# Performance work log

Measured on AMD Instinct MI355X. Metric: run time of the kernel, lower is better.

Reference implementation:

```python
import math
import jax, jax.numpy as jnp
import numpy as np

CAPACITY_FACTOR = 1.0
MIN_CAPACITY = 4


def setup_inputs() -> dict:
    key = jax.random.key(0)
    k1, k2 = jax.random.split(key)
    x = jax.random.normal(k1, (8192, 1024), dtype=jnp.float32)
    wg = jax.random.normal(k2, (1024, 64), dtype=jnp.float32) * 0.02
    return {"x": x, "wg": wg}


def reference(x, wg):
    # Gate projection: [S, D] @ [D, E] -> [S, E]
    logits = x @ wg
    S, E = logits.shape
    # _capacity: ceil(S / E * capacity_factor * 2) for top-2, floored at min_capacity (static)
    capacity = max(math.ceil((S / E) * (CAPACITY_FACTOR * 2.0)), MIN_CAPACITY)

    gates = jax.nn.softmax(logits, axis=-1)           # [S, E]
    org_gates = gates

    # top-1 expert
    indices1_s = jnp.argmax(gates, axis=1)
    mask1 = jax.nn.one_hot(indices1_s, E, dtype=jnp.int32)
    # top-2 expert (deterministic: no gumbel sampling)
    logits_except1 = jnp.where(mask1.astype(bool), -jnp.inf, logits)
    indices2_s = jnp.argmax(logits_except1, axis=1)
    mask2 = jax.nn.one_hot(indices2_s, E, dtype=jnp.int32)

    # per-expert running positions
    locations1 = jnp.cumsum(mask1, axis=0) - 1        # [S, E]
    locations2 = jnp.cumsum(mask2, axis=0) - 1 + jnp.sum(mask1, axis=0, keepdims=True)

    # load-balancing aux loss
    me = jnp.mean(gates, axis=0)
    ce = jnp.mean(mask1.astype(gates.dtype), axis=0)
    l_aux = jnp.sum(me * ce) * E * E

    exp_counts = jnp.sum(mask1 + mask2, axis=0)

    # drop tokens over capacity
    mask1 = mask1 * (locations1 < capacity).astype(jnp.int32)
    mask2 = mask2 * (locations2 < capacity).astype(jnp.int32)

    locations1_s = jnp.sum(locations1 * mask1, axis=1)  # [S]
    locations2_s = jnp.sum(locations2 * mask2, axis=1)

    mask1_f = mask1.astype(gates.dtype)
    mask2_f = mask2.astype(gates.dtype)
    gates1_s = jnp.sum(gates * mask1_f, axis=1)
    gates2_s = jnp.sum(gates * mask2_f, axis=1)
    denom_s = jnp.clip(gates1_s + gates2_s, jnp.finfo(gates.dtype).eps)
    gates1_s = gates1_s / denom_s
    gates2_s = gates2_s / denom_s

    gates1 = gates1_s[:, None] * mask1_f              # [S, E]
    gates2 = gates2_s[:, None] * mask2_f

    locations1_sc = jax.nn.one_hot(locations1_s, capacity, dtype=gates.dtype)  # [S, C]
    locations2_sc = jax.nn.one_hot(locations2_s, capacity, dtype=gates.dtype)

    combine_weights = (jnp.einsum('se,sc->sec', gates1, locations1_sc)
                       + jnp.einsum('se,sc->sec', gates2, locations2_sc))  # [S, E, C]
    dispatch_mask = combine_weights.astype(bool)
    return l_aux, combine_weights, dispatch_mask, exp_counts, org_gates
```

## Files before the change

### kernel.cpp

```cpp
#include <hip/hip_runtime.h>
#include <math.h>

#define S_TOKENS 8192
#define D_DIM    1024
#define E_EXP    64
#define CAPACITY 256
#define TPB      32
#define NCHUNK   (S_TOKENS / TPB)

typedef float fx4 __attribute__((ext_vector_type(4)));

#define SZ_COMBINE   (134217728LL)
#define OFF_COMBINE  (1LL)
#define OFF_DISPATCH (OFF_COMBINE + SZ_COMBINE)
#define OFF_EXPCNT   (OFF_DISPATCH + SZ_COMBINE)
#define OFF_ORGGATES (OFF_EXPCNT + E_EXP)

#define WS_IDX1 0
#define WS_IDX2 (WS_IDX1 + S_TOKENS)
#define WS_G1   (WS_IDX2 + S_TOKENS)
#define WS_G2   (WS_G1 + S_TOKENS)
#define WS_CNT1 (WS_G2 + S_TOKENS)
#define WS_CNT2 (WS_CNT1 + NCHUNK * E_EXP)
#define WS_MEP  (WS_CNT2 + NCHUNK * E_EXP)

__global__ __launch_bounds__(256) void k1_gemm_gate(
    const float* __restrict__ x, const float* __restrict__ wg,
    float* __restrict__ out, int* __restrict__ wsi, float* __restrict__ wsf) {
  const int bid = blockIdx.x;
  const int tid = threadIdx.x;

  __shared__ float xs[32][68];
  __shared__ float ovl[64 * 68];
  __shared__ float mM[32], rS[32];
  __shared__ int   li1[32], li2[32];
  __shared__ float mered[16][64];

  float (*wsh)[64] = (float(*)[64])ovl;
  float (*Lg)[68]  = (float(*)[68])ovl;

  const int tx = tid & 15;
  const int ty = tid >> 4;
  const int s0 = bid * TPB;

  float acc[2][4];
#pragma unroll
  for (int i = 0; i < 2; i++)
#pragma unroll
    for (int q = 0; q < 4; q++) acc[i][q] = 0.f;

  for (int k0 = 0; k0 < D_DIM; k0 += 64) {
#pragma unroll
    for (int r = 0; r < 2; r++) {
      int i = tid + 256 * r;
      int t = i >> 4, c = i & 15;
      *(fx4*)&xs[t][4 * c] =
          *(const fx4*)&x[(size_t)(s0 + t) * D_DIM + k0 + 4 * c];
    }
#pragma unroll
    for (int r = 0; r < 4; r++) {
      int i = tid + 256 * r;
      int t = i >> 4, c = i & 15;
      *(fx4*)&wsh[t][4 * c] =
          *(const fx4*)&wg[(size_t)(k0 + t) * E_EXP + 4 * c];
    }
    __syncthreads();
    for (int kb = 0; kb < 64; kb += 4) {
      fx4 xa[2], wb[4];
#pragma unroll
      for (int i = 0; i < 2; i++) xa[i] = *(fx4*)&xs[ty + 16 * i][kb];
#pragma unroll
      for (int j = 0; j < 4; j++) wb[j] = *(fx4*)&wsh[kb + j][4 * tx];
#pragma unroll
      for (int j = 0; j < 4; j++)
#pragma unroll
        for (int i = 0; i < 2; i++) {
          float xv = xa[i][j];
#pragma unroll
          for (int q = 0; q < 4; q++)
            acc[i][q] = fmaf(xv, wb[j][q], acc[i][q]);
        }
    }
    __syncthreads();
  }

#pragma unroll
  for (int i = 0; i < 2; i++) {
    fx4 v;
#pragma unroll
    for (int q = 0; q < 4; q++) v[q] = acc[i][q];
    *(fx4*)&Lg[ty + 16 * i][4 * tx] = v;
  }
  __syncthreads();

  {
    const int g = tid >> 2;
    const int u = tid & 3;
    if (g < 32) {
      float bv = -INFINITY; int bi = 0;
#pragma unroll
      for (int i = 0; i < 16; i++) {
        int ee = u + 4 * i;
        float v = Lg[g][ee];
        if (v > bv) { bv = v; bi = ee; }
      }
#pragma unroll
      for (int d = 1; d < 4; d <<= 1) {
        float ovv = __shfl_xor(bv, d, 4);
        int   oi  = __shfl_xor(bi, d, 4);
        if (ovv > bv || (ovv == bv && oi < bi)) { bv = ovv; bi = oi; }
      }
      const float m1 = bv; const int i1 = bi;

      float se = 0.f;
#pragma unroll
      for (int i = 0; i < 16; i++) se += expf(Lg[g][u + 4 * i] - m1);
#pragma unroll
      for (int d = 1; d < 4; d <<= 1) se += __shfl_xor(se, d, 4);

      float bv2 = -INFINITY; int bi2 = 0;
#pragma unroll
      for (int i = 0; i < 16; i++) {
        int ee = u + 4 * i;
        float v = Lg[g][ee];
        if (ee != i1 && v > bv2) { bv2 = v; bi2 = ee; }
      }
#pragma unroll
      for (int d = 1; d < 4; d <<= 1) {
        float ovv = __shfl_xor(bv2, d, 4);
        int   oi  = __shfl_xor(bi2, d, 4);
        if (ovv > bv2 || (ovv == bv2 && oi < bi2)) { bv2 = ovv; bi2 = oi; }
      }

      if (u == 0) {
        float rs = 1.0f / se;
        mM[g] = m1; rS[g] = rs;
        li1[g] = i1; li2[g] = bi2;
        int s = s0 + g;
        wsi[WS_IDX1 + s] = i1;
        wsi[WS_IDX2 + s] = bi2;
        wsf[WS_G1 + s] = rs;
        wsf[WS_G2 + s] = expf(bv2 - m1) * rs;
      }
    }
  }
  __syncthreads();

  {
    float ms[4] = {0.f, 0.f, 0.f, 0.f};
#pragma unroll
    for (int i = 0; i < 2; i++) {
      int t = ty + 16 * i;
      float m = mM[t], r = rS[t];
      size_t ob = OFF_ORGGATES + (size_t)(s0 + t) * E_EXP + 4 * tx;
#pragma unroll
      for (int q = 0; q < 4; q++) {
        float gate = expf(Lg[t][4 * tx + q] - m) * r;
        out[ob + q] = gate;
        ms[q] += gate;
      }
    }
#pragma unroll
    for (int q = 0; q < 4; q++) mered[ty][4 * tx + q] = ms[q];
  }
  __syncthreads();

  if (tid < 64) {
    float s = 0.f;
#pragma unroll
    for (int yy = 0; yy < 16; yy++) s += mered[yy][tid];
    wsf[WS_MEP + bid * 64 + tid] = s;
    int c1 = 0, c2 = 0;
    for (int t = 0; t < TPB; t++) {
      c1 += (li1[t] == tid);
      c2 += (li2[t] == tid);
    }
    wsi[WS_CNT1 + bid * 64 + tid] = c1;
    wsi[WS_CNT2 + bid * 64 + tid] = c2;
  }
}

__global__ __launch_bounds__(256) void kB_write(
    float* __restrict__ out, const int* __restrict__ wsi,
    const float* __restrict__ wsf) {
  const int b = blockIdx.x;
  const int tid = threadIdx.x;

  if (b == NCHUNK) {
    if (tid < 64) {
      const int e = tid;
      int t1 = 0, t2 = 0;
      float ms = 0.f;
#pragma unroll 8
      for (int c = 0; c < NCHUNK; c++) {
        t1 += wsi[WS_CNT1 + c * 64 + e];
        t2 += wsi[WS_CNT2 + c * 64 + e];
        ms += wsf[WS_MEP + c * 64 + e];
      }
      out[OFF_EXPCNT + e] = (float)(t1 + t2);
      float me = ms * (1.0f / 8192.0f);
      float ce = (float)t1 * (1.0f / 8192.0f);
      float prod = me * ce * 4096.0f;
#pragma unroll
      for (int d = 1; d < 64; d <<= 1) prod += __shfl_xor(prod, d, 64);
      if (e == 0) out[0] = prod;
    }
    return;
  }

  __shared__ int soff1[64], soff2[64];
  __shared__ int sli1[TPB], sli2[TPB];

  if (tid < TPB) {
    sli1[tid] = wsi[WS_IDX1 + b * TPB + tid];
    sli2[tid] = wsi[WS_IDX2 + b * TPB + tid];
  }
  if (tid < 64) {
    const int e = tid;
    int o1 = 0, o2 = 0, t1 = 0;
#pragma unroll 8
    for (int c = 0; c < NCHUNK; c++) {
      int c1 = wsi[WS_CNT1 + c * 64 + e];
      t1 += c1;
      if (c < b) {
        o1 += c1;
        o2 += wsi[WS_CNT2 + c * 64 + e];
      }
    }
    soff1[e] = o1;
    soff2[e] = t1 + o2;
  }
  __syncthreads();

  bool kept1 = false, kept2 = false;
  size_t o1f = 0, o2f = 0;
  float w1 = 0.f, w2 = 0.f;
  if (tid < TPB) {
    const int t = tid;
    const int e1 = sli1[t], e2 = sli2[t];
    int r1 = 0, r2 = 0;
    for (int j = 0; j < t; j++) {
      r1 += (sli1[j] == e1);
      r2 += (sli2[j] == e2);
    }
    const int loc1 = soff1[e1] + r1;
    const int loc2 = soff2[e2] + r2;
    const int s = b * TPB + t;

    const float g1r = wsf[WS_G1 + s];
    const float g2r = wsf[WS_G2 + s];
    const bool d1 = (loc1 >= CAPACITY);
    const bool d2 = (loc2 >= CAPACITY);
    const float g1f = d1 ? 0.f : g1r;
    const float g2f = d2 ? 0.f : g2r;
    const float denom = fmaxf(g1f + g2f, 1.1920929e-7f);
    w1 = g1f / denom;
    w2 = g2f / denom;
    kept1 = !d1;
    kept2 = !d2;
    o1f = OFF_COMBINE + (size_t)s * (E_EXP * CAPACITY) +
          (size_t)e1 * CAPACITY + loc1;
    o2f = OFF_COMBINE + (size_t)s * (E_EXP * CAPACITY) +
          (size_t)e2 * CAPACITY + loc2;
  }

  {
    const size_t RB = (size_t)TPB * E_EXP * CAPACITY;
    const size_t base = (size_t)b * RB;
    fx4* cb4 = (fx4*)(out + base + 4);
    fx4* db4 = cb4 + (SZ_COMBINE / 4);
    const fx4 z = (fx4)0.f;
#pragma unroll 4
    for (int r = 0; r < 512; r++) {
      int m = tid + 256 * r;
      if (m < 131071) {
        cb4[m] = z;
        db4[m] = z;
      }
    }
    if (tid < 3) {
      out[base + 1 + tid] = 0.f;
      out[SZ_COMBINE + base + 1 + tid] = 0.f;
    } else if (tid == 3) {
      out[base + RB] = 0.f;
      out[SZ_COMBINE + base + RB] = 0.f;
    }
  }
  __syncthreads();

  if (tid < TPB) {
    if (kept1) {
      out[o1f] = w1;
      out[o1f + SZ_COMBINE] = (w1 != 0.f) ? 1.f : 0.f;
    }
    if (kept2) {
      out[o2f] = w2;
      out[o2f + SZ_COMBINE] = (w2 != 0.f) ? 1.f : 0.f;
    }
  }
}

extern "C" void kernel_launch(void* const* d_in, const int* in_sizes, int n_in,
                              void* d_out, int out_size, void* d_ws,
                              size_t ws_size, hipStream_t stream) {
  const float* x  = (const float*)d_in[0];
  const float* wg = (const float*)d_in[1];
  float* out = (float*)d_out;
  int*   wsi = (int*)d_ws;
  float* wsf = (float*)d_ws;

  hipLaunchKernelGGL(k1_gemm_gate, dim3(NCHUNK), dim3(256), 0, stream,
                     x, wg, out, wsi, wsf);
  hipLaunchKernelGGL(kB_write, dim3(NCHUNK + 1), dim3(256), 0, stream,
                     out, wsi, wsf);
}
```

Before: 1.170 ms.

## Zero outputs with hipMemsetAsync and parallelize per-expert prefix scan across 4 warps

Moves zeroing of the large combine and dispatch buffers out of the scatter kernel into a hipMemsetAsync issued before the gate kernel, so the second kernel only scatters the nonzero entries. The per-expert prefix sums over chunk counts are split across four thread groups of 64 with a shared-memory reduction instead of one 64-thread loop over all chunks. The memset also covers l_aux and exp_counts, which are rewritten later, so a little extra is zeroed. The total bytes zeroed stay about the same; the gain depends on whether the driver memset fills memory faster than the in-kernel stores.

```diff
diff --git a/kernel.cpp b/kernel.cpp
--- a/kernel.cpp
+++ b/kernel.cpp
@@ -180,30 +180,41 @@
   }
 }
 
-__global__ __launch_bounds__(256) void kB_write(
+__global__ __launch_bounds__(256) void kB_scan_scatter(
     float* __restrict__ out, const int* __restrict__ wsi,
     const float* __restrict__ wsf) {
   const int b = blockIdx.x;
   const int tid = threadIdx.x;
+  const int e = tid & 63;
+  const int p = tid >> 6;
+
+  __shared__ int pA[4][64];
+  __shared__ int pB[4][64];
+  __shared__ int pC[4][64];
+  __shared__ float pM[4][64];
 
   if (b == NCHUNK) {
+    int a1 = 0, a2 = 0; float ms = 0.f;
+    const int c0 = p * 64;
+#pragma unroll 8
+    for (int i = 0; i < 64; i++) {
+      a1 += wsi[WS_CNT1 + (c0 + i) * 64 + e];
+      a2 += wsi[WS_CNT2 + (c0 + i) * 64 + e];
+      ms += wsf[WS_MEP + (c0 + i) * 64 + e];
+    }
+    pA[p][e] = a1; pB[p][e] = a2; pM[p][e] = ms;
+    __syncthreads();
     if (tid < 64) {
-      const int e = tid;
-      int t1 = 0, t2 = 0;
-      float ms = 0.f;
-#pragma unroll 8
-      for (int c = 0; c < NCHUNK; c++) {
-        t1 += wsi[WS_CNT1 + c * 64 + e];
-        t2 += wsi[WS_CNT2 + c * 64 + e];
-        ms += wsf[WS_MEP + c * 64 + e];
-      }
-      out[OFF_EXPCNT + e] = (float)(t1 + t2);
-      float me = ms * (1.0f / 8192.0f);
+      int t1 = pA[0][tid] + pA[1][tid] + pA[2][tid] + pA[3][tid];
+      int t2 = pB[0][tid] + pB[1][tid] + pB[2][tid] + pB[3][tid];
+      float msum = pM[0][tid] + pM[1][tid] + pM[2][tid] + pM[3][tid];
+      out[OFF_EXPCNT + tid] = (float)(t1 + t2);
+      float me = msum * (1.0f / 8192.0f);
       float ce = (float)t1 * (1.0f / 8192.0f);
       float prod = me * ce * 4096.0f;
 #pragma unroll
       for (int d = 1; d < 64; d <<= 1) prod += __shfl_xor(prod, d, 64);
-      if (e == 0) out[0] = prod;
+      if (tid == 0) out[0] = prod;
     }
     return;
   }
@@ -215,26 +226,31 @@
     sli1[tid] = wsi[WS_IDX1 + b * TPB + tid];
     sli2[tid] = wsi[WS_IDX2 + b * TPB + tid];
   }
+
+  {
+    int a1 = 0, q1 = 0, q2 = 0;
+    const int c0 = p * 64;
+    const int lim = b - c0;
+#pragma unroll 8
+    for (int i = 0; i < 64; i++) {
+      int c1 = wsi[WS_CNT1 + (c0 + i) * 64 + e];
+      int c2 = wsi[WS_CNT2 + (c0 + i) * 64 + e];
+      a1 += c1;
+      if (i < lim) { q1 += c1; q2 += c2; }
+    }
+    pA[p][e] = a1; pB[p][e] = q1; pC[p][e] = q2;
+  }
+  __syncthreads();
+
   if (tid < 64) {
-    const int e = tid;
-    int o1 = 0, o2 = 0, t1 = 0;
-#pragma unroll 8
-    for (int c = 0; c < NCHUNK; c++) {
-      int c1 = wsi[WS_CNT1 + c * 64 + e];
-      t1 += c1;
-      if (c < b) {
-        o1 += c1;
-        o2 += wsi[WS_CNT2 + c * 64 + e];
-      }
-    }
-    soff1[e] = o1;
-    soff2[e] = t1 + o2;
-  }
-  __syncthreads();
-
-  bool kept1 = false, kept2 = false;
-  size_t o1f = 0, o2f = 0;
-  float w1 = 0.f, w2 = 0.f;
+    int t1 = pA[0][tid] + pA[1][tid] + pA[2][tid] + pA[3][tid];
+    int o1 = pB[0][tid] + pB[1][tid] + pB[2][tid] + pB[3][tid];
+    int o2 = pC[0][tid] + pC[1][tid] + pC[2][tid] + pC[3][tid];
+    soff1[tid] = o1;
+    soff2[tid] = t1 + o2;
+  }
+  __syncthreads();
+
   if (tid < TPB) {
     const int t = tid;
     const int e1 = sli1[t], e2 = sli2[t];
@@ -254,48 +270,20 @@
     const float g1f = d1 ? 0.f : g1r;
     const float g2f = d2 ? 0.f : g2r;
     const float denom = fmaxf(g1f + g2f, 1.1920929e-7f);
-    w1 = g1f / denom;
-    w2 = g2f / denom;
-    kept1 = !d1;
-    kept2 = !d2;
-    o1f = OFF_COMBINE + (size_t)s * (E_EXP * CAPACITY) +
-          (size_t)e1 * CAPACITY + loc1;
-    o2f = OFF_COMBINE + (size_t)s * (E_EXP * CAPACITY) +
-          (size_t)e2 * CAPACITY + loc2;
-  }
-
-  {
-    const size_t RB = (size_t)TPB * E_EXP * CAPACITY;
-    const size_t base = (size_t)b * RB;
-    fx4* cb4 = (fx4*)(out + base + 4);
-    fx4* db4 = cb4 + (SZ_COMBINE / 4);
-    const fx4 z = (fx4)0.f;
-#pragma unroll 4
-    for (int r = 0; r < 512; r++) {
-      int m = tid + 256 * r;
-      if (m < 131071) {
-        cb4[m] = z;
-        db4[m] = z;
-      }
-    }
-    if (tid < 3) {
-      out[base + 1 + tid] = 0.f;
-      out[SZ_COMBINE + base + 1 + tid] = 0.f;
-    } else if (tid == 3) {
-      out[base + RB] = 0.f;
-      out[SZ_COMBINE + base + RB] = 0.f;
-    }
-  }
-  __syncthreads();
-
-  if (tid < TPB) {
-    if (kept1) {
-      out[o1f] = w1;
-      out[o1f + SZ_COMBINE] = (w1 != 0.f) ? 1.f : 0.f;
-    }
-    if (kept2) {
-      out[o2f] = w2;
-      out[o2f + SZ_COMBINE] = (w2 != 0.f) ? 1.f : 0.f;
+    const float w1 = g1f / denom;
+    const float w2 = g2f / denom;
+
+    if (!d1) {
+      size_t o = OFF_COMBINE + (size_t)s * (E_EXP * CAPACITY) +
+                 (size_t)e1 * CAPACITY + loc1;
+      out[o] = w1;
+      out[o + SZ_COMBINE] = (w1 != 0.f) ? 1.f : 0.f;
+    }
+    if (!d2) {
+      size_t o = OFF_COMBINE + (size_t)s * (E_EXP * CAPACITY) +
+                 (size_t)e2 * CAPACITY + loc2;
+      out[o] = w2;
+      out[o + SZ_COMBINE] = (w2 != 0.f) ? 1.f : 0.f;
     }
   }
 }
@@ -309,8 +297,10 @@
   int*   wsi = (int*)d_ws;
   float* wsf = (float*)d_ws;
 
+  hipMemsetAsync(out, 0, (size_t)OFF_ORGGATES * sizeof(float), stream);
+
   hipLaunchKernelGGL(k1_gemm_gate, dim3(NCHUNK), dim3(256), 0, stream,
                      x, wg, out, wsi, wsf);
-  hipLaunchKernelGGL(kB_write, dim3(NCHUNK + 1), dim3(256), 0, stream,
+  hipLaunchKernelGGL(kB_scan_scatter, dim3(NCHUNK + 1), dim3(256), 0, stream,
                      out, wsi, wsf);
 }
```

Result: faster. 1.084 ms (-7.3%).
